# Kernel tuning notes

Measured on AMD Instinct MI355X. Metric: run time of the kernel, lower is better.

The kernel has to match this reference:

```python
import jax, jax.numpy as jnp
import numpy as np

N_NODES = 1000
NODE_DIM = 40
SEQ_LEN = 12
IN_FEAT = 32
HID = 64
LAYERS = 3
GDEP = 2
TOPK = 20
TANH_ALPHA = 3.0
PROP_ALPHA = 0.05
LN_EPS = 1e-5


def setup_inputs() -> dict:
    key = jax.random.key(0)
    ks = jax.random.split(key, 20)
    s = 0.1  # weight init scale
    B = 64
    return {
        "x": jax.random.normal(ks[0], (B, N_NODES, SEQ_LEN, IN_FEAT), jnp.float32),
        # graph constructor params
        "emb1": jax.random.normal(ks[1], (N_NODES, NODE_DIM), jnp.float32) * s,
        "emb2": jax.random.normal(ks[2], (N_NODES, NODE_DIM), jnp.float32) * s,
        "lin1_w": jax.random.normal(ks[3], (NODE_DIM, NODE_DIM), jnp.float32) * s,
        "lin1_b": jnp.zeros((NODE_DIM,), jnp.float32),
        "lin2_w": jax.random.normal(ks[4], (NODE_DIM, NODE_DIM), jnp.float32) * s,
        "lin2_b": jnp.zeros((NODE_DIM,), jnp.float32),
        # LSTM (pytorch gate order i,f,g,o)
        "Wih": jax.random.normal(ks[5], (4 * HID, IN_FEAT), jnp.float32) * s,
        "Whh": jax.random.normal(ks[6], (4 * HID, HID), jnp.float32) * s,
        "bih": jnp.zeros((4 * HID,), jnp.float32),
        "bhh": jnp.zeros((4 * HID,), jnp.float32),
        # per-layer linear 64 -> seq_length
        "lin_w": jax.random.normal(ks[7], (LAYERS, SEQ_LEN, HID), jnp.float32) * s,
        "lin_b": jnp.zeros((LAYERS, SEQ_LEN), jnp.float32),
        # mixprop 1: (gdep+1)*12 -> 32
        "mp1_w": jax.random.normal(ks[8], (LAYERS, 32, (GDEP + 1) * SEQ_LEN), jnp.float32) * s,
        "mp1_b": jnp.zeros((LAYERS, 32), jnp.float32),
        # mixprop 2: (gdep+1)*32 -> node_dim
        "mp2_w": jax.random.normal(ks[9], (LAYERS, NODE_DIM, (GDEP + 1) * 32), jnp.float32) * s,
        "mp2_b": jnp.zeros((LAYERS, NODE_DIM), jnp.float32),
        # layernorm affine over (node_dim, N)
        "gamma": jnp.ones((LAYERS, NODE_DIM, N_NODES), jnp.float32),
        "beta": jnp.zeros((LAYERS, NODE_DIM, N_NODES), jnp.float32),
    }


def _graph_constructor(emb1, emb2, lin1_w, lin1_b, lin2_w, lin2_b):
    m1 = jnp.tanh(TANH_ALPHA * (emb1 @ lin1_w.T + lin1_b))
    m2 = jnp.tanh(TANH_ALPHA * (emb2 @ lin2_w.T + lin2_b))
    a = jax.nn.relu(jnp.tanh(TANH_ALPHA * (m1 @ m2.T - m2 @ m1.T)))
    _, idx = jax.lax.top_k(a, TOPK)  # keep top-k neighbors per row
    mask = jnp.zeros_like(a).at[jnp.arange(a.shape[0])[:, None], idx].set(1.0)
    return a * mask


def _lstm_last(x, Wih, Whh, bih, bhh):
    # x: (B, T, IN_FEAT) -> last hidden state (B, HID)
    B = x.shape[0]
    h0 = jnp.zeros((B, HID), x.dtype)
    c0 = jnp.zeros((B, HID), x.dtype)

    def step(carry, xt):
        h, c = carry
        g = xt @ Wih.T + h @ Whh.T + bih + bhh
        i, f, gg, o = jnp.split(g, 4, axis=-1)
        c = jax.nn.sigmoid(f) * c + jax.nn.sigmoid(i) * jnp.tanh(gg)
        h = jax.nn.sigmoid(o) * jnp.tanh(c)
        return (h, c), None

    (h, _), _ = jax.lax.scan(step, (h0, c0), jnp.swapaxes(x, 0, 1))
    return h


def _mixprop(h, adj_norm, w, b):
    # h: (B, C, N); adj_norm: (N, N) row-normalized (adj + I)
    x0 = h
    outs = [h]
    for _ in range(GDEP):
        h = PROP_ALPHA * x0 + (1.0 - PROP_ALPHA) * jnp.einsum('bcw,vw->bcv', h, adj_norm)
        outs.append(h)
    ho = jnp.concatenate(outs, axis=1)  # (B, C*(GDEP+1), N)
    return jnp.einsum('bcn,oc->bon', ho, w) + b[None, :, None]


def _layernorm(h, gamma, beta):
    # normalize over (C, N) dims
    mu = jnp.mean(h, axis=(1, 2), keepdims=True)
    var = jnp.var(h, axis=(1, 2), keepdims=True)
    return (h - mu) * jax.lax.rsqrt(var + LN_EPS) * gamma[None] + beta[None]


def reference(x, emb1, emb2, lin1_w, lin1_b, lin2_w, lin2_b,
              Wih, Whh, bih, bhh, lin_w, lin_b,
              mp1_w, mp1_b, mp2_w, mp2_b, gamma, beta):
    B, N, T, F = x.shape
    adj = _graph_constructor(emb1, emb2, lin1_w, lin1_b, lin2_w, lin2_b)
    adj = adj + jnp.eye(N, dtype=adj.dtype)
    adj_norm = adj / jnp.sum(adj, axis=1, keepdims=True)

    out = _lstm_last(x.reshape(B * N, T, F), Wih, Whh, bih, bhh)  # (B*N, 64)

    h = None
    for j in range(LAYERS):
        hj = out @ lin_w[j].T + lin_b[j]                # (B*N, 12)
        hj = hj.reshape(B, N, SEQ_LEN).transpose(0, 2, 1)  # (B, 12, N)
        hj = jax.nn.relu(_mixprop(hj, adj_norm, mp1_w[j], mp1_b[j]))
        # dropout is identity in eval mode
        hj = _mixprop(hj, adj_norm, mp2_w[j], mp2_b[j])  # (B, node_dim, N)
        h = _layernorm(hj, gamma[j], beta[j])

    return h.transpose(0, 2, 1).reshape(B, N * NODE_DIM)
```

## Files before the change

### kernel.cpp

```cpp
#include <hip/hip_runtime.h>


typedef unsigned short u16;
typedef __attribute__((ext_vector_type(8))) short bf16x8;
typedef __attribute__((ext_vector_type(4))) float fx4;

#define NB 64
#define NNODE 1000
#define TT 12
#define FF 32
#define HH 64
#define DD 40
#define TOPK_ 20
#define EPR2 22

__device__ __forceinline__ float rcp_f(float x) { return __builtin_amdgcn_rcpf(x); }
__device__ __forceinline__ float tanh_f(float x) {
  return fmaf(-2.0f, rcp_f(__expf(2.0f * x) + 1.0f), 1.0f);
}
__device__ __forceinline__ unsigned int cvt_pk(float lo, float hi) {
  unsigned int r;
  asm("v_cvt_pk_bf16_f32 %0, %1, %2" : "=v"(r) : "v"(lo), "v"(hi));
  return r;
}
__device__ __forceinline__ bf16x8 cvt8(const float* p) {
  union { unsigned int u[4]; bf16x8 v; } r;
  #pragma unroll
  for (int e = 0; e < 4; e++) r.u[e] = cvt_pk(p[2 * e], p[2 * e + 1]);
  return r.v;
}
__device__ __forceinline__ bf16x8 cvt8v(float4 a, float4 b) {
  union { unsigned int u[4]; bf16x8 v; } r;
  r.u[0] = cvt_pk(a.x, a.y); r.u[1] = cvt_pk(a.z, a.w);
  r.u[2] = cvt_pk(b.x, b.y); r.u[3] = cvt_pk(b.z, b.w);
  return r.v;
}

__global__ __launch_bounds__(256, 2)
void k_lstm(const float* __restrict__ x, const float* __restrict__ Wih,
            const float* __restrict__ Whh, const float* __restrict__ bih,
            const float* __restrict__ bhh, const float* __restrict__ lw2,
            const float* __restrict__ lb2, float* __restrict__ hj,
            const float* __restrict__ emb1, const float* __restrict__ emb2,
            const float* __restrict__ w1, const float* __restrict__ b1,
            const float* __restrict__ w2, const float* __restrict__ b2,
            float* __restrict__ m1, float* __restrict__ m2,
            const float* __restrict__ p1w, const float* __restrict__ p1b,
            const float* __restrict__ p2w, const float* __restrict__ p2b,
            float* __restrict__ wt) {
  int tid = threadIdx.x;
  if (blockIdx.x >= 1000) {
    int mb = blockIdx.x - 1000;
    if (mb == 313) {
      for (int i = tid; i < 1152; i += 256) { int c = i / 32, o = i % 32; wt[784 + i] = p1w[o * 36 + c]; }
      if (tid < 32) wt[1936 + tid] = p1b[tid];
      for (int i = tid; i < 3840; i += 256) { int c = i / 40, o = i % 40; wt[1968 + i] = p2w[o * 96 + c]; }
      if (tid < 40) wt[5808 + tid] = p2b[tid];
      return;
    }
    int id = mb * 256 + tid;
    if (id >= 2 * NNODE * DD) return;
    int sel = id / (NNODE * DD);
    int r = id % (NNODE * DD);
    int i = r / DD, o = r % DD;
    const float4* emb = (const float4*)((sel ? emb2 : emb1) + i * DD);
    const float4* w = (const float4*)((sel ? w2 : w1) + o * DD);
    float s = (sel ? b2 : b1)[o];
    #pragma unroll
    for (int k4 = 0; k4 < DD / 4; k4++) {
      float4 a = emb[k4], b = w[k4];
      s = fmaf(a.x, b.x, s); s = fmaf(a.y, b.y, s);
      s = fmaf(a.z, b.z, s); s = fmaf(a.w, b.w, s);
    }
    (sel ? m2 : m1)[r] = tanh_f(3.0f * s);
    return;
  }
  __shared__ __align__(16) u16 whf[2 * 16 * 64 * 8];
  __shared__ __align__(16) u16 hsh[4][16][64];
  __shared__ float lwsh[12 * 64];
  __shared__ float lbsh[12];
  int wave = tid >> 6, lane = tid & 63;
  int arow = lane & 15, kg = lane >> 4;

  for (int cc = tid; cc < 2 * 16 * 64; cc += 256) {
    int l = cc & 63, t16 = cc >> 6, ks = t16 >> 4, nt = t16 & 15;
    int row = (nt >> 2) * 64 + (l & 15) * 4 + (nt & 3);
    *(bf16x8*)&whf[cc * 8] = cvt8(Whh + row * 64 + ks * 32 + (l >> 4) * 8);
  }
  for (int i = tid; i < 768; i += 256) lwsh[i] = lw2[i];
  if (tid < 12) lbsh[tid] = lb2[tid];
  __syncthreads();

  bf16x8 wi[16];
  float biasv[16];
  #pragma unroll
  for (int nt = 0; nt < 16; nt++) {
    int row = (nt >> 2) * 64 + arow * 4 + (nt & 3);
    wi[nt] = cvt8(Wih + row * 32 + kg * 8);
    biasv[nt] = bih[row] + bhh[row];
  }

  int seq_base = blockIdx.x * 64 + wave * 16;
  const float* xb = x + (size_t)(seq_base + arow) * (TT * FF) + kg * 8;
  float cst[16];
  #pragma unroll
  for (int q = 0; q < 16; q++) cst[q] = 0.f;

  float4 xf0 = *(const float4*)(xb);
  float4 xf1 = *(const float4*)(xb + 4);

  auto STEP = [&](int t, bool first, float (&hq)[16]) {
    unsigned int zo = 0;
    asm volatile("" : "+v"(zo));
    bf16x8 xa = cvt8v(xf0, xf1);
    if (t < TT - 1) {
      xf0 = *(const float4*)(xb + (t + 1) * FF);
      xf1 = *(const float4*)(xb + (t + 1) * FF + 4);
    }
    fx4 acc[16];
    #pragma unroll
    for (int nt = 0; nt < 16; nt++)
      acc[nt] = (fx4){biasv[nt], biasv[nt], biasv[nt], biasv[nt]};
    #pragma unroll
    for (int nt = 0; nt < 16; nt++)
      acc[nt] = __builtin_amdgcn_mfma_f32_16x16x32_bf16(xa, wi[nt], acc[nt], 0, 0, 0);
    if (!first) {
      asm volatile("" ::: "memory");
      bf16x8 ha0 = *(const bf16x8*)&hsh[wave][arow][kg * 8];
      bf16x8 ha1 = *(const bf16x8*)&hsh[wave][arow][32 + kg * 8];
      asm volatile("" ::: "memory");
      #pragma unroll
      for (int nt = 0; nt < 16; nt++) {
        bf16x8 wb = *(const bf16x8*)&whf[(nt * 64 + lane) * 8 + zo];
        acc[nt] = __builtin_amdgcn_mfma_f32_16x16x32_bf16(ha0, wb, acc[nt], 0, 0, 0);
      }
      #pragma unroll
      for (int nt = 0; nt < 16; nt++) {
        bf16x8 wb = *(const bf16x8*)&whf[((16 + nt) * 64 + lane) * 8 + zo];
        acc[nt] = __builtin_amdgcn_mfma_f32_16x16x32_bf16(ha1, wb, acc[nt], 0, 0, 0);
      }
    }
    #pragma unroll
    for (int i = 0; i < 4; i++) {
      #pragma unroll
      for (int njt = 0; njt < 4; njt++) {
        float iv = acc[njt][i], fv = acc[njt + 4][i];
        float gv = acc[njt + 8][i], ov = acc[njt + 12][i];
        float cpv = cst[i * 4 + njt];
        float ei = __expf(-iv), ef = __expf(-fv);
        float eg = __expf(2.0f * gv), eo = __expf(-ov);
        float A = 1.0f + ef;
        float B = (1.0f + ei) * (eg + 1.0f);
        float c = fmaf(cpv, B, (eg - 1.0f) * A) * rcp_f(A * B);
        cst[i * 4 + njt] = c;
        float ec = __expf(2.0f * c);
        hq[i * 4 + njt] = (ec - 1.0f) * rcp_f((ec + 1.0f) * (1.0f + eo));
      }
    }
  };

  #pragma unroll 1
  for (int t = 0; t < TT - 1; t++) {
    float hq[16];
    STEP(t, t == 0, hq);
    #pragma unroll
    for (int i = 0; i < 4; i++) {
      unsigned int p0 = cvt_pk(hq[i * 4 + 0], hq[i * 4 + 1]);
      unsigned int p1 = cvt_pk(hq[i * 4 + 2], hq[i * 4 + 3]);
      *(uint2*)&hsh[wave][kg * 4 + i][arow * 4] = make_uint2(p0, p1);
    }
  }
  float hq[16];
  STEP(TT - 1, false, hq);

  #pragma unroll
  for (int i = 0; i < 4; i++) {
    float a[12];
    #pragma unroll
    for (int s = 0; s < 12; s++) a[s] = 0.f;
    #pragma unroll
    for (int njt = 0; njt < 4; njt++) {
      float hv = hq[i * 4 + njt];
      #pragma unroll
      for (int s = 0; s < 12; s++)
        a[s] = fmaf(hv, lwsh[s * 64 + arow * 4 + njt], a[s]);
    }
    #pragma unroll
    for (int off = 1; off < 16; off <<= 1) {
      #pragma unroll
      for (int s = 0; s < 12; s++) a[s] += __shfl_xor(a[s], off);
    }
    float outv = a[0];
    #pragma unroll
    for (int s = 1; s < 12; s++) outv = (arow == s) ? a[s] : outv;
    if (arow < 12) {
      int gseq = seq_base + kg * 4 + i;
      int bb = gseq / 1000, nn = gseq - bb * 1000;
      hj[(size_t)(bb * 12 + arow) * NNODE + nn] = outv + lbsh[arow];
    }
  }
}

__global__ void k_adj(const float* __restrict__ m1, const float* __restrict__ m2,
                      int2* __restrict__ pae) {
  int v0 = blockIdx.x * 4, tid = threadIdx.x;
  int lane = tid & 63, wave = tid >> 6;
  __shared__ float arow4[4][1024];
  __shared__ float m1v4[4][DD], m2v4[4][DD];
  for (int i = tid; i < 4 * DD; i += 256) {
    int r = i / DD, k = i % DD;
    m1v4[r][k] = m1[(v0 + r) * DD + k];
    m2v4[r][k] = m2[(v0 + r) * DD + k];
  }
  __syncthreads();
  for (int w = tid; w < NNODE; w += 256) {
    const float4* m2r = (const float4*)(m2 + w * DD);
    const float4* m1r = (const float4*)(m1 + w * DD);
    float4 a[10], bb[10];
    #pragma unroll
    for (int k4 = 0; k4 < 10; k4++) { a[k4] = m2r[k4]; bb[k4] = m1r[k4]; }
    #pragma unroll
    for (int r = 0; r < 4; r++) {
      float d1 = 0.f, d2 = 0.f;
      #pragma unroll
      for (int k4 = 0; k4 < 10; k4++) {
        d1 = fmaf(m1v4[r][k4 * 4 + 0], a[k4].x, d1);
        d1 = fmaf(m1v4[r][k4 * 4 + 1], a[k4].y, d1);
        d1 = fmaf(m1v4[r][k4 * 4 + 2], a[k4].z, d1);
        d1 = fmaf(m1v4[r][k4 * 4 + 3], a[k4].w, d1);
        d2 = fmaf(m2v4[r][k4 * 4 + 0], bb[k4].x, d2);
        d2 = fmaf(m2v4[r][k4 * 4 + 1], bb[k4].y, d2);
        d2 = fmaf(m2v4[r][k4 * 4 + 2], bb[k4].z, d2);
        d2 = fmaf(m2v4[r][k4 * 4 + 3], bb[k4].w, d2);
      }
      arow4[r][w] = fmaxf(tanh_f(3.0f * (d1 - d2)), 0.0f);
    }
  }
  __syncthreads();
  int v = v0 + wave, l = lane;
  float rv[16];
  #pragma unroll
  for (int q = 0; q < 16; q++) {
    int idx = q * 64 + l;
    rv[q] = (idx < NNODE) ? arow4[wave][idx] : -2.f;
  }
  float rs = 1.f;
  float myv = 0.f; int myi = 0;
  #pragma unroll
  for (int sel = 0; sel < TOPK_; sel++) {
    float bv = rv[0]; int bi = l;
    #pragma unroll
    for (int q = 1; q < 16; q++) {
      int idx = q * 64 + l;
      if (rv[q] > bv) { bv = rv[q]; bi = idx; }
    }
    #pragma unroll
    for (int off = 1; off < 64; off <<= 1) {
      float ov = __shfl_xor(bv, off); int oi = __shfl_xor(bi, off);
      if (ov > bv || (ov == bv && oi < bi)) { bv = ov; bi = oi; }
    }
    rs += bv;
    if (l == sel + 1) { myv = bv; myi = bi; }
    #pragma unroll
    for (int q = 0; q < 16; q++)
      if (q * 64 + l == bi) rv[q] = -2.f;
  }
  float inv = rcp_f(rs);
  if (l == 0)          pae[v * EPR2] = make_int2(v, __float_as_int(inv));
  else if (l <= TOPK_) pae[v * EPR2 + l] = make_int2(myi, __float_as_int(myv * inv));
  else if (l == 21)    pae[v * EPR2 + 21] = make_int2(v, 0);
}

__global__ void k_prop4(const float* __restrict__ hin, const int2* __restrict__ pae,
                        float* __restrict__ ho, int C) {
  int NG = C >> 2;
  int b = blockIdx.x / NG, g = blockIdx.x % NG;
  int c0 = g * 4;
  __shared__ __align__(16) float r0t[NNODE][4];
  __shared__ __align__(16) float r1t[NNODE][4];
  int tid = threadIdx.x;
  const float* src = hin + ((size_t)b * C + c0) * NNODE;
  float* dst = ho + (size_t)b * 2 * C * NNODE;
  for (int n = tid; n < NNODE; n += 256) {
    float4 v;
    v.x = src[n];
    v.y = src[NNODE + n];
    v.z = src[2 * NNODE + n];
    v.w = src[3 * NNODE + n];
    *(float4*)&r0t[n][0] = v;
  }
  __syncthreads();
  for (int n = tid; n < NNODE; n += 256) {
    const int4* pa4 = (const int4*)(pae + (size_t)n * EPR2);
    float4 s = {0.f, 0.f, 0.f, 0.f};
    #pragma unroll
    for (int e = 0; e < EPR2 / 2; e++) {
      int4 p = pa4[e];
      float av = __int_as_float(p.y);
      float4 rv = *(const float4*)&r0t[p.x][0];
      s.x = fmaf(av, rv.x, s.x); s.y = fmaf(av, rv.y, s.y);
      s.z = fmaf(av, rv.z, s.z); s.w = fmaf(av, rv.w, s.w);
      float aw = __int_as_float(p.w);
      float4 rw = *(const float4*)&r0t[p.z][0];
      s.x = fmaf(aw, rw.x, s.x); s.y = fmaf(aw, rw.y, s.y);
      s.z = fmaf(aw, rw.z, s.z); s.w = fmaf(aw, rw.w, s.w);
    }
    float4 x0 = *(const float4*)&r0t[n][0];
    float4 h1;
    h1.x = fmaf(0.95f, s.x, 0.05f * x0.x);
    h1.y = fmaf(0.95f, s.y, 0.05f * x0.y);
    h1.z = fmaf(0.95f, s.z, 0.05f * x0.z);
    h1.w = fmaf(0.95f, s.w, 0.05f * x0.w);
    *(float4*)&r1t[n][0] = h1;
    dst[(size_t)(c0 + 0) * NNODE + n] = h1.x;
    dst[(size_t)(c0 + 1) * NNODE + n] = h1.y;
    dst[(size_t)(c0 + 2) * NNODE + n] = h1.z;
    dst[(size_t)(c0 + 3) * NNODE + n] = h1.w;
  }
  __syncthreads();
  for (int n = tid; n < NNODE; n += 256) {
    const int4* pa4 = (const int4*)(pae + (size_t)n * EPR2);
    float4 s = {0.f, 0.f, 0.f, 0.f};
    #pragma unroll
    for (int e = 0; e < EPR2 / 2; e++) {
      int4 p = pa4[e];
      float av = __int_as_float(p.y);
      float4 rv = *(const float4*)&r1t[p.x][0];
      s.x = fmaf(av, rv.x, s.x); s.y = fmaf(av, rv.y, s.y);
      s.z = fmaf(av, rv.z, s.z); s.w = fmaf(av, rv.w, s.w);
      float aw = __int_as_float(p.w);
      float4 rw = *(const float4*)&r1t[p.z][0];
      s.x = fmaf(aw, rw.x, s.x); s.y = fmaf(aw, rw.y, s.y);
      s.z = fmaf(aw, rw.z, s.z); s.w = fmaf(aw, rw.w, s.w);
    }
    float4 x0 = *(const float4*)&r0t[n][0];
    dst[(size_t)(C + c0 + 0) * NNODE + n] = fmaf(0.95f, s.x, 0.05f * x0.x);
    dst[(size_t)(C + c0 + 1) * NNODE + n] = fmaf(0.95f, s.y, 0.05f * x0.y);
    dst[(size_t)(C + c0 + 2) * NNODE + n] = fmaf(0.95f, s.z, 0.05f * x0.z);
    dst[(size_t)(C + c0 + 3) * NNODE + n] = fmaf(0.95f, s.w, 0.05f * x0.w);
  }
}

template <int C1, int COUT>
__global__ void k_proj(const float* __restrict__ src0, const float* __restrict__ src12,
                       const float* __restrict__ wt, const float* __restrict__ bb,
                       float* __restrict__ out, int relu) {
  int id = blockIdx.x * 256 + threadIdx.x;
  int b = id / NNODE, n = id % NNODE;
  float acc[COUT];
  #pragma unroll
  for (int o = 0; o < COUT; o++) acc[o] = bb[o];
  for (int c = 0; c < C1; c++) {
    float hv = src0[(size_t)(b * C1 + c) * NNODE + n];
    #pragma unroll
    for (int o = 0; o < COUT; o++) acc[o] = fmaf(hv, wt[c * COUT + o], acc[o]);
  }
  for (int c = 0; c < 2 * C1; c++) {
    float hv = src12[(size_t)(b * 2 * C1 + c) * NNODE + n];
    #pragma unroll
    for (int o = 0; o < COUT; o++) acc[o] = fmaf(hv, wt[(C1 + c) * COUT + o], acc[o]);
  }
  #pragma unroll
  for (int o = 0; o < COUT; o++) {
    float vv = acc[o];
    if (relu) vv = fmaxf(vv, 0.f);
    out[(size_t)(b * COUT + o) * NNODE + n] = vv;
  }
}

__global__ void k_ln(const float* __restrict__ hj2, const float* __restrict__ gamma,
                     const float* __restrict__ beta, float* __restrict__ out) {
  int b = blockIdx.x, tid = threadIdx.x, lane = tid & 63, wave = tid >> 6;
  const float* base = hj2 + (size_t)b * DD * NNODE;
  const float4* p = (const float4*)base;
  float s = 0.f, q = 0.f;
  for (int i = tid; i < DD * NNODE / 4; i += 1024) {
    float4 vv = p[i];
    s += vv.x + vv.y + vv.z + vv.w;
    q = fmaf(vv.x, vv.x, q); q = fmaf(vv.y, vv.y, q);
    q = fmaf(vv.z, vv.z, q); q = fmaf(vv.w, vv.w, q);
  }
  for (int off = 32; off; off >>= 1) { s += __shfl_down(s, off); q += __shfl_down(q, off); }
  __shared__ float ss[16], sq[16];
  __shared__ float smu, srstd;
  if (lane == 0) { ss[wave] = s; sq[wave] = q; }
  __syncthreads();
  if (tid == 0) {
    const float invN = 1.0f / (float)(DD * NNODE);
    float S = 0.f, Q = 0.f;
    for (int t = 0; t < 16; t++) { S += ss[t]; Q += sq[t]; }
    float mu = S * invN;
    float var = Q * invN - mu * mu;
    smu = mu; srstd = __builtin_amdgcn_rsqf(var + 1e-5f);
  }
  __syncthreads();
  float mu = smu, rstd = srstd;
  if (tid >= NNODE) return;
  int n = tid;
  size_t obase = (size_t)b * (NNODE * DD) + (size_t)n * DD;
  #pragma unroll
  for (int d0 = 0; d0 < DD / 4; d0++) {
    float tt[4];
    #pragma unroll
    for (int qq = 0; qq < 4; qq++) {
      int d = d0 * 4 + qq;
      float h0 = base[(size_t)d * NNODE + n];
      tt[qq] = (h0 - mu) * rstd * gamma[d * NNODE + n] + beta[d * NNODE + n];
    }
    *(float4*)(out + obase + d0 * 4) = (float4){tt[0], tt[1], tt[2], tt[3]};
  }
}

#define OFF_M1   0
#define OFF_M2   40000
#define OFF_PAE  80000
#define OFF_HJ   124000
#define OFF_HO1  892000
#define OFF_O1   2428000
#define OFF_HO2  4476000
#define OFF_HJ2  8572000
#define OFF_WT   11132000

extern "C" void kernel_launch(void* const* d_in, const int* in_sizes, int n_in,
                              void* d_out, int out_size, void* d_ws, size_t ws_size,
                              hipStream_t stream) {
  (void)in_sizes; (void)n_in; (void)out_size; (void)ws_size;
  const float* x     = (const float*)d_in[0];
  const float* emb1  = (const float*)d_in[1];
  const float* emb2  = (const float*)d_in[2];
  const float* l1w   = (const float*)d_in[3];
  const float* l1b   = (const float*)d_in[4];
  const float* l2w   = (const float*)d_in[5];
  const float* l2b   = (const float*)d_in[6];
  const float* Wih   = (const float*)d_in[7];
  const float* Whh   = (const float*)d_in[8];
  const float* bih   = (const float*)d_in[9];
  const float* bhh   = (const float*)d_in[10];
  const float* lin_w = (const float*)d_in[11];
  const float* lin_b = (const float*)d_in[12];
  const float* mp1w  = (const float*)d_in[13];
  const float* mp1b  = (const float*)d_in[14];
  const float* mp2w  = (const float*)d_in[15];
  const float* mp2b  = (const float*)d_in[16];
  const float* gamma = (const float*)d_in[17];
  const float* beta  = (const float*)d_in[18];

  float* ws   = (float*)d_ws;
  float* m1   = ws + OFF_M1;
  float* m2   = ws + OFF_M2;
  int2*  pae  = (int2*)(ws + OFF_PAE);
  float* hj   = ws + OFF_HJ;
  float* ho1  = ws + OFF_HO1;
  float* o1   = ws + OFF_O1;
  float* ho2  = ws + OFF_HO2;
  float* hj2  = ws + OFF_HJ2;
  float* wt   = ws + OFF_WT;

  k_lstm<<<dim3(1314), dim3(256), 0, stream>>>(x, Wih, Whh, bih, bhh,
                                               lin_w + 1536, lin_b + 24, hj,
                                               emb1, emb2, l1w, l1b, l2w, l2b, m1, m2,
                                               mp1w + 2304, mp1b + 64,
                                               mp2w + 7680, mp2b + 80, wt);
  k_adj<<<dim3(250), dim3(256), 0, stream>>>(m1, m2, pae);
  k_prop4<<<dim3(64 * 3), dim3(256), 0, stream>>>(hj, pae, ho1, 12);
  k_proj<12, 32><<<dim3(250), dim3(256), 0, stream>>>(hj, ho1, wt + 784, wt + 1936, o1, 1);
  k_prop4<<<dim3(64 * 8), dim3(256), 0, stream>>>(o1, pae, ho2, 32);
  k_proj<32, 40><<<dim3(250), dim3(256), 0, stream>>>(o1, ho2, wt + 1968, wt + 5808, hj2, 0);
  k_ln<<<dim3(NB), dim3(1024), 0, stream>>>(hj2, gamma + 80000, beta + 80000,
                                            (float*)d_out);
}
```

Before: 249.3 us.

## Split layernorm into partial-stats and apply kernels; use SoA shared layout in prop

```diff
diff --git a/kernel.cpp b/kernel.cpp
--- a/kernel.cpp
+++ b/kernel.cpp
@@ -276,68 +276,59 @@
   int NG = C >> 2;
   int b = blockIdx.x / NG, g = blockIdx.x % NG;
   int c0 = g * 4;
-  __shared__ __align__(16) float r0t[NNODE][4];
-  __shared__ __align__(16) float r1t[NNODE][4];
+  __shared__ float r0c[4][1024];
+  __shared__ float r1c[4][1024];
   int tid = threadIdx.x;
   const float* src = hin + ((size_t)b * C + c0) * NNODE;
   float* dst = ho + (size_t)b * 2 * C * NNODE;
   for (int n = tid; n < NNODE; n += 256) {
-    float4 v;
-    v.x = src[n];
-    v.y = src[NNODE + n];
-    v.z = src[2 * NNODE + n];
-    v.w = src[3 * NNODE + n];
-    *(float4*)&r0t[n][0] = v;
+    r0c[0][n] = src[n];
+    r0c[1][n] = src[NNODE + n];
+    r0c[2][n] = src[2 * NNODE + n];
+    r0c[3][n] = src[3 * NNODE + n];
   }
   __syncthreads();
   for (int n = tid; n < NNODE; n += 256) {
     const int4* pa4 = (const int4*)(pae + (size_t)n * EPR2);
-    float4 s = {0.f, 0.f, 0.f, 0.f};
+    float s0 = 0.f, s1 = 0.f, s2 = 0.f, s3 = 0.f;
     #pragma unroll
     for (int e = 0; e < EPR2 / 2; e++) {
       int4 p = pa4[e];
       float av = __int_as_float(p.y);
-      float4 rv = *(const float4*)&r0t[p.x][0];
-      s.x = fmaf(av, rv.x, s.x); s.y = fmaf(av, rv.y, s.y);
-      s.z = fmaf(av, rv.z, s.z); s.w = fmaf(av, rv.w, s.w);
+      s0 = fmaf(av, r0c[0][p.x], s0); s1 = fmaf(av, r0c[1][p.x], s1);
+      s2 = fmaf(av, r0c[2][p.x], s2); s3 = fmaf(av, r0c[3][p.x], s3);
       float aw = __int_as_float(p.w);
-      float4 rw = *(const float4*)&r0t[p.z][0];
-      s.x = fmaf(aw, rw.x, s.x); s.y = fmaf(aw, rw.y, s.y);
-      s.z = fmaf(aw, rw.z, s.z); s.w = fmaf(aw, rw.w, s.w);
-    }
-    float4 x0 = *(const float4*)&r0t[n][0];
-    float4 h1;
-    h1.x = fmaf(0.95f, s.x, 0.05f * x0.x);
-    h1.y = fmaf(0.95f, s.y, 0.05f * x0.y);
-    h1.z = fmaf(0.95f, s.z, 0.05f * x0.z);
-    h1.w = fmaf(0.95f, s.w, 0.05f * x0.w);
-    *(float4*)&r1t[n][0] = h1;
-    dst[(size_t)(c0 + 0) * NNODE + n] = h1.x;
-    dst[(size_t)(c0 + 1) * NNODE + n] = h1.y;
-    dst[(size_t)(c0 + 2) * NNODE + n] = h1.z;
-    dst[(size_t)(c0 + 3) * NNODE + n] = h1.w;
+      s0 = fmaf(aw, r0c[0][p.z], s0); s1 = fmaf(aw, r0c[1][p.z], s1);
+      s2 = fmaf(aw, r0c[2][p.z], s2); s3 = fmaf(aw, r0c[3][p.z], s3);
+    }
+    float h10 = fmaf(0.95f, s0, 0.05f * r0c[0][n]);
+    float h11 = fmaf(0.95f, s1, 0.05f * r0c[1][n]);
+    float h12 = fmaf(0.95f, s2, 0.05f * r0c[2][n]);
+    float h13 = fmaf(0.95f, s3, 0.05f * r0c[3][n]);
+    r1c[0][n] = h10; r1c[1][n] = h11; r1c[2][n] = h12; r1c[3][n] = h13;
+    dst[(size_t)(c0 + 0) * NNODE + n] = h10;
+    dst[(size_t)(c0 + 1) * NNODE + n] = h11;
+    dst[(size_t)(c0 + 2) * NNODE + n] = h12;
+    dst[(size_t)(c0 + 3) * NNODE + n] = h13;
   }
   __syncthreads();
   for (int n = tid; n < NNODE; n += 256) {
     const int4* pa4 = (const int4*)(pae + (size_t)n * EPR2);
-    float4 s = {0.f, 0.f, 0.f, 0.f};
+    float s0 = 0.f, s1 = 0.f, s2 = 0.f, s3 = 0.f;
     #pragma unroll
     for (int e = 0; e < EPR2 / 2; e++) {
       int4 p = pa4[e];
       float av = __int_as_float(p.y);
-      float4 rv = *(const float4*)&r1t[p.x][0];
-      s.x = fmaf(av, rv.x, s.x); s.y = fmaf(av, rv.y, s.y);
-      s.z = fmaf(av, rv.z, s.z); s.w = fmaf(av, rv.w, s.w);
+      s0 = fmaf(av, r1c[0][p.x], s0); s1 = fmaf(av, r1c[1][p.x], s1);
+      s2 = fmaf(av, r1c[2][p.x], s2); s3 = fmaf(av, r1c[3][p.x], s3);
       float aw = __int_as_float(p.w);
-      float4 rw = *(const float4*)&r1t[p.z][0];
-      s.x = fmaf(aw, rw.x, s.x); s.y = fmaf(aw, rw.y, s.y);
-      s.z = fmaf(aw, rw.z, s.z); s.w = fmaf(aw, rw.w, s.w);
-    }
-    float4 x0 = *(const float4*)&r0t[n][0];
-    dst[(size_t)(C + c0 + 0) * NNODE + n] = fmaf(0.95f, s.x, 0.05f * x0.x);
-    dst[(size_t)(C + c0 + 1) * NNODE + n] = fmaf(0.95f, s.y, 0.05f * x0.y);
-    dst[(size_t)(C + c0 + 2) * NNODE + n] = fmaf(0.95f, s.z, 0.05f * x0.z);
-    dst[(size_t)(C + c0 + 3) * NNODE + n] = fmaf(0.95f, s.w, 0.05f * x0.w);
+      s0 = fmaf(aw, r1c[0][p.z], s0); s1 = fmaf(aw, r1c[1][p.z], s1);
+      s2 = fmaf(aw, r1c[2][p.z], s2); s3 = fmaf(aw, r1c[3][p.z], s3);
+    }
+    dst[(size_t)(C + c0 + 0) * NNODE + n] = fmaf(0.95f, s0, 0.05f * r0c[0][n]);
+    dst[(size_t)(C + c0 + 1) * NNODE + n] = fmaf(0.95f, s1, 0.05f * r0c[1][n]);
+    dst[(size_t)(C + c0 + 2) * NNODE + n] = fmaf(0.95f, s2, 0.05f * r0c[2][n]);
+    dst[(size_t)(C + c0 + 3) * NNODE + n] = fmaf(0.95f, s3, 0.05f * r0c[3][n]);
   }
 }
 
@@ -368,35 +359,38 @@
   }
 }
 
-__global__ void k_ln(const float* __restrict__ hj2, const float* __restrict__ gamma,
-                     const float* __restrict__ beta, float* __restrict__ out) {
-  int b = blockIdx.x, tid = threadIdx.x, lane = tid & 63, wave = tid >> 6;
-  const float* base = hj2 + (size_t)b * DD * NNODE;
-  const float4* p = (const float4*)base;
+__global__ void k_lnpart(const float* __restrict__ hj2, float* __restrict__ part) {
+  int b = blockIdx.x >> 2, qt = blockIdx.x & 3;
+  int tid = threadIdx.x, lane = tid & 63, wave = tid >> 6;
+  const float4* p = (const float4*)(hj2 + (size_t)b * DD * NNODE) + qt * 2500;
   float s = 0.f, q = 0.f;
-  for (int i = tid; i < DD * NNODE / 4; i += 1024) {
+  for (int i = tid; i < 2500; i += 256) {
     float4 vv = p[i];
     s += vv.x + vv.y + vv.z + vv.w;
     q = fmaf(vv.x, vv.x, q); q = fmaf(vv.y, vv.y, q);
     q = fmaf(vv.z, vv.z, q); q = fmaf(vv.w, vv.w, q);
   }
   for (int off = 32; off; off >>= 1) { s += __shfl_down(s, off); q += __shfl_down(q, off); }
-  __shared__ float ss[16], sq[16];
-  __shared__ float smu, srstd;
+  __shared__ float ss[4], sq[4];
   if (lane == 0) { ss[wave] = s; sq[wave] = q; }
   __syncthreads();
   if (tid == 0) {
-    const float invN = 1.0f / (float)(DD * NNODE);
-    float S = 0.f, Q = 0.f;
-    for (int t = 0; t < 16; t++) { S += ss[t]; Q += sq[t]; }
-    float mu = S * invN;
-    float var = Q * invN - mu * mu;
-    smu = mu; srstd = __builtin_amdgcn_rsqf(var + 1e-5f);
-  }
-  __syncthreads();
-  float mu = smu, rstd = srstd;
-  if (tid >= NNODE) return;
-  int n = tid;
+    part[b * 8 + qt] = (ss[0] + ss[1]) + (ss[2] + ss[3]);
+    part[b * 8 + 4 + qt] = (sq[0] + sq[1]) + (sq[2] + sq[3]);
+  }
+}
+
+__global__ void k_lnapply(const float* __restrict__ hj2, const float* __restrict__ part,
+                          const float* __restrict__ gamma, const float* __restrict__ beta,
+                          float* __restrict__ out) {
+  int id = blockIdx.x * 256 + threadIdx.x;
+  int b = id / NNODE, n = id % NNODE;
+  float S = (part[b * 8 + 0] + part[b * 8 + 1]) + (part[b * 8 + 2] + part[b * 8 + 3]);
+  float Q = (part[b * 8 + 4] + part[b * 8 + 5]) + (part[b * 8 + 6] + part[b * 8 + 7]);
+  const float invN = 1.0f / (float)(DD * NNODE);
+  float mu = S * invN;
+  float var = Q * invN - mu * mu;
+  float rstd = __builtin_amdgcn_rsqf(var + 1e-5f);
   size_t obase = (size_t)b * (NNODE * DD) + (size_t)n * DD;
   #pragma unroll
   for (int d0 = 0; d0 < DD / 4; d0++) {
@@ -404,7 +398,7 @@
     #pragma unroll
     for (int qq = 0; qq < 4; qq++) {
       int d = d0 * 4 + qq;
-      float h0 = base[(size_t)d * NNODE + n];
+      float h0 = hj2[(size_t)(b * DD + d) * NNODE + n];
       tt[qq] = (h0 - mu) * rstd * gamma[d * NNODE + n] + beta[d * NNODE + n];
     }
     *(float4*)(out + obase + d0 * 4) = (float4){tt[0], tt[1], tt[2], tt[3]};
@@ -419,7 +413,8 @@
 #define OFF_O1   2428000
 #define OFF_HO2  4476000
 #define OFF_HJ2  8572000
-#define OFF_WT   11132000
+#define OFF_PART 11132000
+#define OFF_WT   11132512
 
 extern "C" void kernel_launch(void* const* d_in, const int* in_sizes, int n_in,
                               void* d_out, int out_size, void* d_ws, size_t ws_size,
@@ -454,6 +449,7 @@
   float* o1   = ws + OFF_O1;
   float* ho2  = ws + OFF_HO2;
   float* hj2  = ws + OFF_HJ2;
+  float* part = ws + OFF_PART;
   float* wt   = ws + OFF_WT;
 
   k_lstm<<<dim3(1314), dim3(256), 0, stream>>>(x, Wih, Whh, bih, bhh,
@@ -466,6 +462,7 @@
   k_proj<12, 32><<<dim3(250), dim3(256), 0, stream>>>(hj, ho1, wt + 784, wt + 1936, o1, 1);
   k_prop4<<<dim3(64 * 8), dim3(256), 0, stream>>>(o1, pae, ho2, 32);
   k_proj<32, 40><<<dim3(250), dim3(256), 0, stream>>>(o1, ho2, wt + 1968, wt + 5808, hj2, 0);
-  k_ln<<<dim3(NB), dim3(1024), 0, stream>>>(hj2, gamma + 80000, beta + 80000,
-                                            (float*)d_out);
-}
+  k_lnpart<<<dim3(NB * 4), dim3(256), 0, stream>>>(hj2, part);
+  k_lnapply<<<dim3(250), dim3(256), 0, stream>>>(hj2, part, gamma + 80000, beta + 80000,
+                                                 (float*)d_out);
+}
```

Result: no change. 250.7 us, median of 2 (+0.6%).
